# Kernel tuning notes

Hardware: AMD Instinct MI355X
Metric: run time of the kernel (lower is better)

Reference implementation:

```python
import jax, jax.numpy as jnp
import numpy as np

B, S, T = 16, 400, 51
V, E, H = 50000, 128, 256
MAX_OOV = 50
EXT = V + MAX_OOV
COV_LOSS_WEIGHT = 1.0


def setup_inputs() -> dict:
    key = jax.random.key(0)
    ks = jax.random.split(key, 24)
    sc = 0.05  # param scale
    inp = {
        "tgt": jax.random.randint(ks[0], (B, T), 0, V, dtype=jnp.int32),
        "hidden": jax.random.normal(ks[1], (1, B, H), jnp.float32),
        "cell": jax.random.normal(ks[2], (1, B, H), jnp.float32),
        "encoder_outputs": jax.random.normal(ks[3], (B, S, H), jnp.float32),
        "src_lens": jax.random.randint(ks[4], (B,), S // 2, S + 1, dtype=jnp.int32),
        "src_ids": jax.random.randint(ks[5], (B, S), 0, V, dtype=jnp.int32),
        # -1 means in-vocab token; >=0 means OOV slot index (max MAX_OOV-1)
        "src_oov_map": jax.random.randint(ks[6], (B, S), -1, MAX_OOV, dtype=jnp.int32),
        "embedding": jax.random.normal(ks[7], (V, E), jnp.float32) * sc,
        "W_h": jax.random.normal(ks[8], (H, H), jnp.float32) * sc,
        "W_s": jax.random.normal(ks[9], (H, H), jnp.float32) * sc,
        "w_c": jax.random.normal(ks[10], (H,), jnp.float32) * sc,
        "v": jax.random.normal(ks[11], (H,), jnp.float32) * sc,
        "b_attn": jnp.zeros((1,), jnp.float32),
        "W_ih": jax.random.normal(ks[12], (4 * H, E + H), jnp.float32) * sc,
        "W_hh": jax.random.normal(ks[13], (4 * H, H), jnp.float32) * sc,
        "b_ih": jax.random.normal(ks[14], (4 * H,), jnp.float32) * sc,
        "b_hh": jax.random.normal(ks[15], (4 * H,), jnp.float32) * sc,
        "W_pg": jax.random.normal(ks[16], (1, 2 * H + E), jnp.float32) * sc,
        "b_pg": jnp.zeros((1,), jnp.float32),
        "W_out": jax.random.normal(ks[17], (V, 2 * H), jnp.float32) * sc,
        "b_out": jnp.zeros((V,), jnp.float32),
    }
    return inp


def reference(tgt, hidden, cell, encoder_outputs, src_lens, src_ids, src_oov_map,
              embedding, W_h, W_s, w_c, v, b_attn,
              W_ih, W_hh, b_ih, b_hh, W_pg, b_pg, W_out, b_out):
    # Precompute encoder projection and masks (loop-invariant)
    Wh_h = jnp.einsum('bsh,kh->bsk', encoder_outputs, W_h)        # [B,S,H]
    pad_mask = jnp.arange(S)[None, :] >= src_lens[:, None]       # [B,S]
    copy_idx = jnp.where(src_oov_map >= 0, V + src_oov_map, src_ids)  # [B,S]
    batch_idx = jnp.arange(B)[:, None]

    def step(carry, y_prev):
        h, c, cov = carry                                       # [B,H],[B,H],[B,S]
        emb = embedding[y_prev]                                 # [B,E]
        # coverage attention (additive, See et al. 2017 eq. 9-11)
        attn_in = Wh_h + (h @ W_s.T)[:, None, :] + cov[..., None] * w_c + b_attn
        scores = jnp.tanh(attn_in) @ v                          # [B,S]
        scores = jnp.where(pad_mask, -1e9, scores)
        attn = jax.nn.softmax(scores, axis=1)                   # [B,S]
        context = jnp.einsum('bs,bsh->bh', attn, encoder_outputs)
        cov_loss = jnp.sum(jnp.minimum(attn, cov), axis=1)      # [B]
        # single-layer LSTM cell (torch gate order i,f,g,o)
        x = jnp.concatenate([emb, context], axis=1)             # [B,E+H]
        gates = x @ W_ih.T + h @ W_hh.T + b_ih + b_hh
        i, f, g, o = jnp.split(gates, 4, axis=1)
        c_new = jax.nn.sigmoid(f) * c + jax.nn.sigmoid(i) * jnp.tanh(g)
        h_new = jax.nn.sigmoid(o) * jnp.tanh(c_new)
        # pointer-generator mixture
        p_gen = jax.nn.sigmoid(
            jnp.concatenate([h_new, context, emb], axis=1) @ W_pg.T + b_pg)  # [B,1]
        logits = jnp.concatenate([h_new, context], axis=1) @ W_out.T + b_out
        vocab_dist = jax.nn.softmax(logits, axis=1)             # [B,V]
        ext_dist = jnp.pad(vocab_dist, ((0, 0), (0, MAX_OOV)))  # [B,EXT]
        copy_dist = jnp.zeros((B, EXT), vocab_dist.dtype).at[batch_idx, copy_idx].add(attn)
        final = p_gen * ext_dist + (1.0 - p_gen) * copy_dist
        return (h_new, c_new, cov + attn), (final, cov_loss)

    carry0 = (hidden[0], cell[0], jnp.zeros((B, S), jnp.float32))
    # teacher forcing: decoder input at step t is tgt[:, t-1], t = 1..T-1
    (hT, cT, _), (dists, cov_losses) = jax.lax.scan(step, carry0, tgt[:, :-1].T)
    all_dists = jnp.transpose(dists, (1, 0, 2))                 # [B,T-1,EXT]
    coverage_loss = COV_LOSS_WEIGHT * jnp.mean(cov_losses)
    return all_dists, hT[None], cT[None], coverage_loss
```

## Files before the change

### kernel.cpp

```cpp
#include <hip/hip_runtime.h>
#include <math.h>

#define CB 16
#define CS 400
#define CT 51
#define CTM1 50
#define CV 50000
#define CE 128
#define CH 256
#define CMAXOOV 50
#define CEXT (CV + CMAXOOV)
#define CX 640
#define NST 16
#define NGT 16
#define NWK 223
#define NBLK 256
#define NTILE 782

typedef __attribute__((ext_vector_type(4))) float f32x4;
typedef __attribute__((ext_vector_type(8))) short short8;
typedef unsigned int U32;
typedef unsigned long long U64;

__device__ __forceinline__ float wave_sum(float x) {
#pragma unroll
  for (int o = 32; o > 0; o >>= 1) x += __shfl_xor(x, o);
  return x;
}
__device__ __forceinline__ float sigm(float x) {
  return 1.f / (1.f + __expf(-x));
}
__device__ __forceinline__ float ftanh(float x) {
  x = fminf(fmaxf(x, -15.f), 15.f);
  float e = __expf(2.f * x);
  return (e - 1.f) / (e + 1.f);
}
__device__ __forceinline__ unsigned short f2bf(float f) {
  union { float f; U32 u; } x;
  x.f = f;
  U32 r = x.u + 0x7FFFu + ((x.u >> 16) & 1u);
  return (unsigned short)(r >> 16);
}
__device__ __forceinline__ float bf2f(unsigned short u) {
  return __uint_as_float(((U32)u) << 16);
}
__device__ __forceinline__ U64 pack4(float a, float b, float c, float d) {
  return (U64)f2bf(a) | ((U64)f2bf(b) << 16) | ((U64)f2bf(c) << 32) |
         ((U64)f2bf(d) << 48);
}
__device__ __forceinline__ U32 ald32(const U32* p) {
  return __hip_atomic_load(p, __ATOMIC_RELAXED, __HIP_MEMORY_SCOPE_AGENT);
}
__device__ __forceinline__ void ast32(U32* p, U32 v) {
  __hip_atomic_store(p, v, __ATOMIC_RELAXED, __HIP_MEMORY_SCOPE_AGENT);
}
__device__ __forceinline__ void ast64(U64* p, U64 v) {
  __hip_atomic_store(p, v, __ATOMIC_RELAXED, __HIP_MEMORY_SCOPE_AGENT);
}
#define VM0 asm volatile("s_waitcnt vmcnt(0)" ::: "memory")

__global__ __launch_bounds__(256) void pw_convert(
    const float* __restrict__ W, unsigned short* __restrict__ Wb) {
  size_t i = ((size_t)blockIdx.x * 256 + threadIdx.x) * 8;
  float4 a = *(const float4*)(W + i);
  float4 b = *(const float4*)(W + i + 4);
  short8 o;
  o[0] = (short)f2bf(a.x); o[1] = (short)f2bf(a.y);
  o[2] = (short)f2bf(a.z); o[3] = (short)f2bf(a.w);
  o[4] = (short)f2bf(b.x); o[5] = (short)f2bf(b.y);
  o[6] = (short)f2bf(b.z); o[7] = (short)f2bf(b.w);
  *(short8*)(Wb + i) = o;
}

__global__ __launch_bounds__(256) void pw_cat(
    const float* __restrict__ W_ih, const float* __restrict__ W_hh,
    unsigned short* __restrict__ Wcat) {
  int t8 = blockIdx.x * 256 + threadIdx.x;
  int j = t8 / 80, k8 = t8 % 80;
  short8 o;
#pragma unroll
  for (int i = 0; i < 8; ++i) {
    int k = k8 * 8 + i;
    float v = (k < CE + CH) ? W_ih[(size_t)j * (CE + CH) + k]
                            : W_hh[(size_t)j * CH + (k - (CE + CH))];
    o[i] = (short)f2bf(v);
  }
  *(short8*)(Wcat + (size_t)t8 * 8) = o;
}

__global__ __launch_bounds__(256) void pw_t256(const float* __restrict__ in,
                                               float* __restrict__ out) {
  int j = blockIdx.x, k = threadIdx.x;
  out[j * CH + k] = in[k * CH + j];
}

__global__ __launch_bounds__(256) void pw_t256_bf16(
    const float* __restrict__ in, unsigned short* __restrict__ out) {
  int j = blockIdx.x, k = threadIdx.x;
  out[j * CH + k] = f2bf(in[k * CH + j]);
}

__global__ __launch_bounds__(256) void pw_cvt16(
    const float* __restrict__ in, unsigned short* __restrict__ out) {
  size_t i = ((size_t)blockIdx.x * 256 + threadIdx.x) * 8;
  float4 a = *(const float4*)(in + i);
  float4 b = *(const float4*)(in + i + 4);
  short8 o;
  o[0] = (short)f2bf(a.x); o[1] = (short)f2bf(a.y);
  o[2] = (short)f2bf(a.z); o[3] = (short)f2bf(a.w);
  o[4] = (short)f2bf(b.x); o[5] = (short)f2bf(b.y);
  o[6] = (short)f2bf(b.z); o[7] = (short)f2bf(b.w);
  *(short8*)(out + i) = o;
}

__global__ __launch_bounds__(256) void p0_precompute(
    const float* __restrict__ enc, const float* __restrict__ W_hT,
    const int* __restrict__ src_ids, const int* __restrict__ src_oov,
    unsigned short* __restrict__ Wh_h16, int* __restrict__ copy_idx) {
  const int row0 = blockIdx.x * 8, tid = threadIdx.x;
  __shared__ float erT[CH * 8];
#pragma unroll
  for (int i = 0; i < 8; ++i) {
    int idx = tid + i * 256;
    int r = idx >> 8, j = idx & 255;
    erT[j * 8 + r] = enc[(size_t)row0 * CH + idx];
  }
  if (tid < 8) {
    int row = row0 + tid;
    int ov = src_oov[row];
    copy_idx[row] = (ov >= 0) ? (CV + ov) : src_ids[row];
  }
  __syncthreads();
  float acc[8] = {0, 0, 0, 0, 0, 0, 0, 0};
#pragma unroll 4
  for (int j = 0; j < CH; ++j) {
    float w = W_hT[j * CH + tid];
    float4 e0 = *(const float4*)&erT[j * 8];
    float4 e1 = *(const float4*)&erT[j * 8 + 4];
    acc[0] += e0.x * w; acc[1] += e0.y * w; acc[2] += e0.z * w; acc[3] += e0.w * w;
    acc[4] += e1.x * w; acc[5] += e1.y * w; acc[6] += e1.z * w; acc[7] += e1.w * w;
  }
#pragma unroll
  for (int r = 0; r < 8; ++r)
    Wh_h16[(size_t)(row0 + r) * CH + tid] = f2bf(acc[r]);
}

__global__ __launch_bounds__(256) void z_init(U32* __restrict__ ctrl,
                                              float* __restrict__ part) {
  int tid = blockIdx.x * 256 + threadIdx.x;
  if (tid < 2048) ctrl[tid] = 0u;
  for (int i = tid; i < CTM1 * CB * 64; i += 256 * 64) part[i] = 0.f;
}

__global__ __launch_bounds__(1024, 4) void mega(
    const int* __restrict__ tgt, const float* __restrict__ hidden,
    const float* __restrict__ cell, const int* __restrict__ src_lens,
    const float* __restrict__ embedding, const float* __restrict__ w_c,
    const float* __restrict__ v_vec, const float* __restrict__ b_attn,
    const float* __restrict__ b_ih, const float* __restrict__ b_hh,
    const float* __restrict__ W_pg, const float* __restrict__ b_pg,
    const float* __restrict__ b_out,
    const unsigned short* __restrict__ Wh_h16,
    const unsigned short* __restrict__ enc16,
    const unsigned short* __restrict__ W_sT16,
    const unsigned short* __restrict__ Wcat,
    const unsigned short* __restrict__ Wb, U64* __restrict__ A64,
    float* __restrict__ HexF, unsigned short* __restrict__ attn16,
    float* __restrict__ p_gen_g, float* __restrict__ part,
    float* __restrict__ covloss_b, U32* __restrict__ ctrl,
    float* __restrict__ dout) {
  const int bid = blockIdx.x, tid = threadIdx.x;
  const int lane = tid & 63, wv = tid >> 6;
  U32* release = ctrl + 256;
  U32* xrdy = ctrl + 1280;
  U32* grdy = ctrl + 1536;

  __shared__ __align__(16) U64 sh_big[2592];
  __shared__ float cov_s[CS];
  __shared__ float a_s[CS];
  __shared__ __align__(16) float h_cur[CH];
  __shared__ float hws_s[CH];
  __shared__ __align__(16) float ctx_s[CH];
  __shared__ float emb_s[CE];
  __shared__ float pctx[4 * CH];
  __shared__ float gsl[4][CB][16];
  __shared__ int sh_tok[CB];
  __shared__ float red[16];
  __shared__ float stat[4];
  __shared__ float prs[16][16];

  if (bid < NST) {
    const int b = bid;
    const int len = src_lens[b];
    const float ba = b_attn[0];
    const int k4 = lane * 4;
    const float4 wc4 = *(const float4*)(w_c + k4);
    const float4 vv4 = *(const float4*)(v_vec + k4);
    const int kg = tid & 255, grp = tid >> 8;
    float covl = 0.f;

    if (tid < CS) cov_s[tid] = 0.f;
    if (tid < CH) h_cur[tid] = hidden[b * CH + tid];
    __syncthreads();
    {
      float acc = 0.f;
#pragma unroll 8
      for (int j = grp * 64; j < grp * 64 + 64; ++j)
        acc += h_cur[j] * bf2f(W_sT16[j * CH + kg]);
      pctx[grp * CH + kg] = acc;
    }
    __syncthreads();
    if (tid < CH)
      hws_s[tid] = pctx[tid] + pctx[CH + tid] + pctx[2 * CH + tid] +
                   pctx[3 * CH + tid];
    __syncthreads();

    for (int t = 0; t < CTM1; ++t) {
      if (t > 0) {
        if (tid < CS) {
          float a = a_s[tid], cv = cov_s[tid];
          covl += fminf(a, cv);
          cov_s[tid] = cv + a;
        }
        __syncthreads();
      }
      float ps = 0.f;
      for (int s = wv; s < CS; s += 16) {
        float cv = cov_s[s];
        U64 wq = *(const U64*)(Wh_h16 + ((size_t)(b * CS + s)) * CH + k4);
        float p =
            ftanh(bf2f((unsigned short)wq) + hws_s[k4] + cv * wc4.x + ba) *
                vv4.x +
            ftanh(bf2f((unsigned short)(wq >> 16)) + hws_s[k4 + 1] +
                  cv * wc4.y + ba) *
                vv4.y +
            ftanh(bf2f((unsigned short)(wq >> 32)) + hws_s[k4 + 2] +
                  cv * wc4.z + ba) *
                vv4.z +
            ftanh(bf2f((unsigned short)(wq >> 48)) + hws_s[k4 + 3] +
                  cv * wc4.w + ba) *
                vv4.w;
        p = wave_sum(p);
        if (lane == 0) {
          float e = (s < len) ? __expf(p) : 0.f;
          a_s[s] = e;
          ps += e;
        }
      }
      if (lane == 0) red[wv] = ps;
      __syncthreads();
      if (tid == 0) {
        float s2 = 0.f;
#pragma unroll
        for (int i = 0; i < 16; ++i) s2 += red[i];
        stat[0] = 1.f / s2;
      }
      __syncthreads();
      const float inv = stat[0];
      if (tid < CS) {
        float a = a_s[tid] * inv;
        a_s[tid] = a;
        attn16[((size_t)t * CB + b) * CS + tid] = f2bf(a);
      }
      __syncthreads();
      {
        float pc = 0.f;
        const unsigned short* er =
            enc16 + ((size_t)(b * CS + grp * 100)) * CH + kg;
#pragma unroll 10
        for (int i = 0; i < 100; ++i)
          pc += a_s[grp * 100 + i] * bf2f(er[(size_t)i * CH]);
        pctx[grp * CH + kg] = pc;
      }
      __syncthreads();
      if (tid < CH)
        ctx_s[tid] = pctx[tid] + pctx[CH + tid] + pctx[2 * CH + tid] +
                     pctx[3 * CH + tid];
      __syncthreads();
      if (tid < 64) {
        ast64(&A64[(size_t)t * 2048 + b * 128 + 64 + tid],
              pack4(ctx_s[4 * tid], ctx_s[4 * tid + 1], ctx_s[4 * tid + 2],
                    ctx_s[4 * tid + 3]));
      }
      VM0;
      __syncthreads();
      if (tid == 0) ast32(&xrdy[b * 16], (U32)(t + 1));
      if (tid < CE)
        emb_s[tid] = embedding[(size_t)tgt[b * CT + t] * CE + tid];
      if (wv == 0) {
        int gg = 0;
        while (gg < (1 << 22)) {
          U32 v = (lane < NGT) ? ald32(&grdy[lane * 16]) : (U32)(t + 1);
          if (__all(v >= (U32)(t + 1))) break;
          __builtin_amdgcn_s_sleep(1);
          ++gg;
        }
      }
      __syncthreads();
      if (tid < CH) h_cur[tid] = HexF[((size_t)t * CB + b) * CH + tid];
      __syncthreads();
      {
        float acc = 0.f;
#pragma unroll 8
        for (int j = grp * 64; j < grp * 64 + 64; ++j)
          acc += h_cur[j] * bf2f(W_sT16[j * CH + kg]);
        pctx[grp * CH + kg] = acc;
      }
      __syncthreads();
      if (tid < CH)
        hws_s[tid] = pctx[tid] + pctx[CH + tid] + pctx[2 * CH + tid] +
                     pctx[3 * CH + tid];
      {
        float z = 0.f;
        if (tid < CH)
          z = h_cur[tid] * W_pg[tid] + ctx_s[tid] * W_pg[CH + tid];
        if (tid < CE) z += emb_s[tid] * W_pg[2 * CH + tid];
        z = wave_sum(z);
        if (lane == 0) red[wv] = z;
        __syncthreads();
        if (tid == 0) {
          float s2 = 0.f;
#pragma unroll
          for (int i = 0; i < 16; ++i) s2 += red[i];
          p_gen_g[t * CB + b] = sigm(s2 + b_pg[0]);
        }
      }
      __syncthreads();
    }
    if (tid < CS) covl += fminf(a_s[tid], cov_s[tid]);
    covl = wave_sum(covl);
    if (lane == 0) red[wv] = covl;
    __syncthreads();
    if (tid == 0) {
      float s2 = 0.f;
#pragma unroll
      for (int i = 0; i < 16; ++i) s2 += red[i];
      covloss_b[b] = s2;
    }
    if (tid < CH) {
      const size_t D0 = (size_t)CB * CTM1 * CEXT;
      dout[D0 + b * CH + tid] = h_cur[tid];
    }
  } else if (bid < NST + NGT) {
    const int g = bid - NST;
    const int nn = lane & 15, gq = lane >> 4;
    U64* xg64 = sh_big;
    short* xg_s = (short*)sh_big;
    const short8* x8 = (const short8*)sh_big;
    const int cb = tid >> 4, cj = tid & 15, cu = g * 16 + (tid & 15);
    float c_reg = 0.f, bi0 = 0.f, bi1 = 0.f, bi2 = 0.f, bi3 = 0.f;
    if (tid < 256) {
      c_reg = cell[cb * CH + cu];
      bi0 = b_ih[cu] + b_hh[cu];
      bi1 = b_ih[CH + cu] + b_hh[CH + cu];
      bi2 = b_ih[2 * CH + cu] + b_hh[2 * CH + cu];
      bi3 = b_ih[3 * CH + cu] + b_hh[3 * CH + cu];
    }
    for (int t = 0; t < CTM1; ++t) {
      if (t > 0 && wv == 0) {
        int gg = 0;
        while (gg < (1 << 22)) {
          U32 v = (lane < NGT) ? ald32(&grdy[lane * 16]) : (U32)t;
          if (__all(v >= (U32)t)) break;
          __builtin_amdgcn_s_sleep(1);
          ++gg;
        }
      }
      if (tid < CB) sh_tok[tid] = tgt[tid * CT + t];
      __syncthreads();
      for (int idx = tid; idx < CB * CE; idx += 1024) {
        int bb = idx >> 7, k = idx & 127;
        xg_s[bb * 648 + k] = (short)f2bf(embedding[(size_t)sh_tok[bb] * CE + k]);
      }
      if (t == 0) {
        for (int idx = tid; idx < CB * CH; idx += 1024) {
          int bb = idx >> 8, k = idx & 255;
          xg_s[bb * 648 + 384 + k] = (short)f2bf(hidden[bb * CH + k]);
        }
      } else {
        if (tid < 1024) {
          int bb = tid >> 6, i = tid & 63;
          xg64[bb * 162 + 96 + i] = A64[(size_t)(t - 1) * 2048 + bb * 128 + i];
        }
      }
      __syncthreads();
      f32x4 acc = {0.f, 0.f, 0.f, 0.f};
      if (wv < 4) {
        const int ncol = wv * 256 + g * 16 + nn;
        const short8* bp = (const short8*)Wcat + (size_t)ncol * 80;
#pragma unroll
        for (int kt = 0; kt < 4; ++kt)
          acc = __builtin_amdgcn_mfma_f32_16x16x32_bf16(
              x8[nn * 81 + kt * 4 + gq], bp[kt * 4 + gq], acc, 0, 0, 0);
#pragma unroll
        for (int kt = 12; kt < 20; ++kt)
          acc = __builtin_amdgcn_mfma_f32_16x16x32_bf16(
              x8[nn * 81 + kt * 4 + gq], bp[kt * 4 + gq], acc, 0, 0, 0);
      }
      if (wv == 0) {
        int gg = 0;
        while (gg < (1 << 22)) {
          U32 v = (lane < NST) ? ald32(&xrdy[lane * 16]) : (U32)(t + 1);
          if (__all(v >= (U32)(t + 1))) break;
          __builtin_amdgcn_s_sleep(1);
          ++gg;
        }
      }
      __syncthreads();
      if (tid < 1024) {
        int bb = tid >> 6, i = tid & 63;
        xg64[bb * 162 + 32 + i] = A64[(size_t)t * 2048 + bb * 128 + 64 + i];
      }
      __syncthreads();
      if (wv < 4) {
        const int ncol = wv * 256 + g * 16 + nn;
        const short8* bp = (const short8*)Wcat + (size_t)ncol * 80;
#pragma unroll
        for (int kt = 4; kt < 12; ++kt)
          acc = __builtin_amdgcn_mfma_f32_16x16x32_bf16(
              x8[nn * 81 + kt * 4 + gq], bp[kt * 4 + gq], acc, 0, 0, 0);
#pragma unroll
        for (int r = 0; r < 4; ++r) gsl[wv][gq * 4 + r][nn] = acc[r];
      }
      __syncthreads();
      if (tid < 256) {
        float gi = gsl[0][cb][cj] + bi0;
        float gf = gsl[1][cb][cj] + bi1;
        float gg2 = gsl[2][cb][cj] + bi2;
        float go = gsl[3][cb][cj] + bi3;
        float cn = sigm(gf) * c_reg + sigm(gi) * ftanh(gg2);
        c_reg = cn;
        float hn = sigm(go) * ftanh(cn);
        ast32((U32*)&HexF[((size_t)t * CB + cb) * CH + cu],
              __float_as_uint(hn));
        float h1 = __shfl_down(hn, 1);
        float h2 = __shfl_down(hn, 2);
        float h3 = __shfl_down(hn, 3);
        if (!(cj & 3))
          ast64(&A64[(size_t)t * 2048 + cb * 128 + (cu >> 2)],
                pack4(hn, h1, h2, h3));
      }
      VM0;
      __syncthreads();
      if (tid == 0) ast32(&grdy[g * 16], (U32)(t + 1));
    }
    if (tid < 256) {
      const size_t D0 = (size_t)CB * CTM1 * CEXT;
      dout[D0 + CB * CH + cb * CH + cu] = c_reg;
    }
  } else if (bid == NST + NGT) {
    for (int t = 0; t < CTM1; ++t) {
      if (wv == 0) {
        int gg = 0;
        while (gg < (1 << 22)) {
          U32 v = (lane < NGT) ? ald32(&grdy[lane * 16]) : (U32)(t + 1);
          if (__all(v >= (U32)(t + 1))) break;
          __builtin_amdgcn_s_sleep(4);
          ++gg;
        }
      }
      __syncthreads();
      if (tid < 64) ast32(&release[tid * 16], (U32)(t + 1));
      __syncthreads();
    }
  } else {
    const int vb = bid - NST - NGT - 1;
    const int rep = vb & 63;
    const int nn = lane & 15, g = lane >> 4;
    const int t4 = (wv >> 2) * NWK + vb;
    const int v = t4 * 64 + (wv & 3) * 16 + nn;
    const bool live = (t4 < NTILE) && (v < CV);
    const int vc = live ? v : CV - 1;
    U64* a64l = sh_big;
    const short8* lds8 = (const short8*)sh_big;
    const short8* bp = (const short8*)Wb + (size_t)vc * 64;
    const float bo = live ? b_out[v] : 0.f;
    for (int t = 0; t < CTM1; ++t) {
      if (tid == 0) {
        int gg = 0;
        while (ald32(&release[rep * 16]) < (U32)(t + 1) && ++gg < (1 << 18))
          __builtin_amdgcn_s_sleep(32);
      }
      __syncthreads();
      {
        const U64* src = A64 + (size_t)t * 2048;
#pragma unroll
        for (int i = 0; i < 2; ++i) {
          int idx = tid + i * 1024;
          int row = idx >> 7, col = idx & 127;
          a64l[row * 130 + col] = src[idx];
        }
      }
      __syncthreads();
      short8 af[16];
#pragma unroll
      for (int kt = 0; kt < 16; ++kt) af[kt] = lds8[nn * 65 + kt * 4 + g];
      f32x4 acc = {0.f, 0.f, 0.f, 0.f};
#pragma unroll
      for (int kt = 0; kt < 16; ++kt)
        acc = __builtin_amdgcn_mfma_f32_16x16x32_bf16(af[kt], bp[kt * 4 + g],
                                                      acc, 0, 0, 0);
      float ev[4];
#pragma unroll
      for (int r = 0; r < 4; ++r) {
        float e = live ? __expf(acc[r] + bo) : 0.f;
        if (live) dout[((size_t)((g * 4 + r) * CTM1 + t)) * CEXT + v] = e;
#pragma unroll
        for (int o = 1; o < 16; o <<= 1) e += __shfl_xor(e, o);
        ev[r] = e;
      }
      if (nn == 0) {
#pragma unroll
        for (int r = 0; r < 4; ++r) prs[wv][g * 4 + r] = ev[r];
      }
      __syncthreads();
      if (tid < 16) {
        float s = 0.f;
#pragma unroll
        for (int w = 0; w < 16; ++w) s += prs[w][tid];
        atomicAdd(&part[((size_t)t * CB + tid) * 64 + rep], s);
      }
      __syncthreads();
    }
  }
}

__global__ __launch_bounds__(256) void post_norm(
    const float* __restrict__ part, const float* __restrict__ p_gen_g,
    float* __restrict__ dout) {
  const int R = blockIdx.x;
  const int b = R / CTM1, t = R % CTM1;
  const int tid = threadIdx.x;
  __shared__ float stat;
  float s = (tid < 64) ? part[((size_t)t * CB + b) * 64 + tid] : 0.f;
  s = wave_sum(s);
  if (tid == 0) stat = p_gen_g[t * CB + b] / s;
  __syncthreads();
  float inv = stat;
  float* drow = dout + (size_t)R * CEXT;
  for (int v = tid; v < CEXT; v += 256)
    drow[v] = (v < CV) ? drow[v] * inv : 0.f;
}

__global__ __launch_bounds__(256) void post_tail(
    const unsigned short* __restrict__ attn16,
    const float* __restrict__ p_gen_g, const int* __restrict__ copy_idx,
    const float* __restrict__ covloss_b, float* __restrict__ dout) {
  const int b = blockIdx.x, tid = threadIdx.x;
  for (int t = 0; t < CTM1; ++t) {
    float pg1 = 1.f - p_gen_g[t * CB + b];
    const unsigned short* ar = attn16 + ((size_t)t * CB + b) * CS;
    float* drow = dout + ((size_t)(b * CTM1 + t)) * CEXT;
    for (int s = tid; s < CS; s += 256)
      atomicAdd(drow + copy_idx[b * CS + s], pg1 * bf2f(ar[s]));
  }
  if (b == 0 && tid == 0) {
    const size_t D0 = (size_t)CB * CTM1 * CEXT;
    float s = 0.f;
    for (int i = 0; i < CB; ++i) s += covloss_b[i];
    dout[D0 + 2 * CB * CH] = s / (float)(CTM1 * CB);
  }
}

extern "C" void kernel_launch(void* const* d_in, const int* in_sizes, int n_in,
                              void* d_out, int out_size, void* d_ws,
                              size_t ws_size, hipStream_t stream) {
  const int* tgt = (const int*)d_in[0];
  const float* hidden = (const float*)d_in[1];
  const float* cell = (const float*)d_in[2];
  const float* enc = (const float*)d_in[3];
  const int* src_lens = (const int*)d_in[4];
  const int* src_ids = (const int*)d_in[5];
  const int* src_oov = (const int*)d_in[6];
  const float* embedding = (const float*)d_in[7];
  const float* W_h = (const float*)d_in[8];
  const float* W_s = (const float*)d_in[9];
  const float* w_c = (const float*)d_in[10];
  const float* v_vec = (const float*)d_in[11];
  const float* b_attn = (const float*)d_in[12];
  const float* W_ih = (const float*)d_in[13];
  const float* W_hh = (const float*)d_in[14];
  const float* b_ih = (const float*)d_in[15];
  const float* b_hh = (const float*)d_in[16];
  const float* W_pg = (const float*)d_in[17];
  const float* b_pg = (const float*)d_in[18];
  const float* W_out = (const float*)d_in[19];
  const float* b_out = (const float*)d_in[20];
  float* dout = (float*)d_out;

  float* ws = (float*)d_ws;
  float* W_hT = ws;
  float* p_gen_g = W_hT + CH * CH;
  float* part = p_gen_g + CTM1 * CB;
  float* covloss_b = part + CTM1 * CB * 64;
  float* HexF = covloss_b + 16;
  int* copy_idx = (int*)(HexF + (size_t)CTM1 * CB * CH);
  U32* ctrl = (U32*)(copy_idx + CB * CS);
  U64* A64 = (U64*)(ctrl + 2048);
  unsigned short* attn16 =
      (unsigned short*)(A64 + (size_t)CTM1 * 2048);
  unsigned short* Wh_h16 = attn16 + (size_t)CTM1 * CB * CS;
  unsigned short* enc16 = Wh_h16 + (size_t)CB * CS * CH;
  unsigned short* W_sT16 = enc16 + (size_t)CB * CS * CH;
  unsigned short* Wcat = W_sT16 + CH * CH;
  unsigned short* Wb = Wcat + (size_t)(4 * CH) * CX;

  z_init<<<64, 256, 0, stream>>>(ctrl, part);
  pw_convert<<<(CV * 2 * CH) / (256 * 8), 256, 0, stream>>>(W_out, Wb);
  pw_cat<<<((4 * CH) * CX / 8) / 256, 256, 0, stream>>>(W_ih, W_hh, Wcat);
  pw_t256<<<CH, CH, 0, stream>>>(W_h, W_hT);
  pw_t256_bf16<<<CH, CH, 0, stream>>>(W_s, W_sT16);
  pw_cvt16<<<(CB * CS * CH) / (256 * 8), 256, 0, stream>>>(enc, enc16);
  p0_precompute<<<CB * CS / 8, 256, 0, stream>>>(enc, W_hT, src_ids, src_oov,
                                                 Wh_h16, copy_idx);

  void* kargs[] = {
      (void*)&tgt,      (void*)&hidden,    (void*)&cell,    (void*)&src_lens,
      (void*)&embedding,(void*)&w_c,       (void*)&v_vec,   (void*)&b_attn,
      (void*)&b_ih,     (void*)&b_hh,      (void*)&W_pg,    (void*)&b_pg,
      (void*)&b_out,    (void*)&Wh_h16,    (void*)&enc16,   (void*)&W_sT16,
      (void*)&Wcat,     (void*)&Wb,        (void*)&A64,     (void*)&HexF,
      (void*)&attn16,   (void*)&p_gen_g,   (void*)&part,    (void*)&covloss_b,
      (void*)&ctrl,     (void*)&dout};
  hipError_t e = hipLaunchCooperativeKernel((const void*)mega, dim3(NBLK),
                                            dim3(1024), kargs, 0, stream);
  if (e != hipSuccess) {
    hipLaunchKernelGGL(mega, dim3(NBLK), dim3(1024), 0, stream, tgt, hidden,
                       cell, src_lens, embedding, w_c, v_vec, b_attn, b_ih,
                       b_hh, W_pg, b_pg, b_out, Wh_h16, enc16, W_sT16, Wcat,
                       Wb, A64, HexF, attn16, p_gen_g, part, covloss_b, ctrl,
                       dout);
  }
  post_norm<<<CB * CTM1, 256, 0, stream>>>(part, p_gen_g, dout);
  post_tail<<<CB, 256, 0, stream>>>(attn16, p_gen_g, copy_idx, covloss_b,
                                    dout);
}
```

Before: 1.862 ms.

## Repartition LSTM gate blocks by batch group and move W_s projection into them

Each LSTM gate block now owns 4 batch rows and 64 hidden units, using all 16 waves for MFMA instead of 4. Each block computes partial h·W_s and h·W_pg products for its slice and publishes them, so attention blocks only sum four partials instead of redoing a 256x256 matvec on the serial critical path. Attention blocks also wait only on the 4 gate blocks that own their batch group rather than on all 16. The cost is extra global traffic for the partial buffers and more per-step work inside the gate blocks.

```diff
diff --git a/kernel.cpp b/kernel.cpp
--- a/kernel.cpp
+++ b/kernel.cpp
@@ -54,6 +54,10 @@
 __device__ __forceinline__ void ast32(U32* p, U32 v) {
   __hip_atomic_store(p, v, __ATOMIC_RELAXED, __HIP_MEMORY_SCOPE_AGENT);
 }
+__device__ __forceinline__ void astf(float* p, float v) {
+  __hip_atomic_store((U32*)p, __float_as_uint(v), __ATOMIC_RELAXED,
+                     __HIP_MEMORY_SCOPE_AGENT);
+}
 __device__ __forceinline__ void ast64(U64* p, U64 v) {
   __hip_atomic_store(p, v, __ATOMIC_RELAXED, __HIP_MEMORY_SCOPE_AGENT);
 }
@@ -165,7 +169,8 @@
     const unsigned short* __restrict__ W_sT16,
     const unsigned short* __restrict__ Wcat,
     const unsigned short* __restrict__ Wb, U64* __restrict__ A64,
-    float* __restrict__ HexF, unsigned short* __restrict__ attn16,
+    float* __restrict__ HexF, float* __restrict__ HwsP,
+    float* __restrict__ PgP, unsigned short* __restrict__ attn16,
     float* __restrict__ p_gen_g, float* __restrict__ part,
     float* __restrict__ covloss_b, U32* __restrict__ ctrl,
     float* __restrict__ dout) {
@@ -183,7 +188,7 @@
   __shared__ __align__(16) float ctx_s[CH];
   __shared__ float emb_s[CE];
   __shared__ float pctx[4 * CH];
-  __shared__ float gsl[4][CB][16];
+  __shared__ float gsl[4][4][64];
   __shared__ int sh_tok[CB];
   __shared__ float red[16];
   __shared__ float stat[4];
@@ -191,6 +196,7 @@
 
   if (bid < NST) {
     const int b = bid;
+    const int gi = b >> 2;
     const int len = src_lens[b];
     const float ba = b_attn[0];
     const int k4 = lane * 4;
@@ -276,6 +282,8 @@
       if (tid < CH)
         ctx_s[tid] = pctx[tid] + pctx[CH + tid] + pctx[2 * CH + tid] +
                      pctx[3 * CH + tid];
+      if (tid < CE)
+        emb_s[tid] = embedding[(size_t)tgt[b * CT + t] * CE + tid];
       __syncthreads();
       if (tid < 64) {
         ast64(&A64[(size_t)t * 2048 + b * 128 + 64 + tid],
@@ -285,45 +293,36 @@
       VM0;
       __syncthreads();
       if (tid == 0) ast32(&xrdy[b * 16], (U32)(t + 1));
-      if (tid < CE)
-        emb_s[tid] = embedding[(size_t)tgt[b * CT + t] * CE + tid];
+      {
+        float z = 0.f;
+        if (tid < CH) z = ctx_s[tid] * W_pg[CH + tid];
+        if (tid < CE) z += emb_s[tid] * W_pg[2 * CH + tid];
+        z = wave_sum(z);
+        if (lane == 0) red[wv] = z;
+      }
+      __syncthreads();
       if (wv == 0) {
         int gg = 0;
         while (gg < (1 << 22)) {
-          U32 v = (lane < NGT) ? ald32(&grdy[lane * 16]) : (U32)(t + 1);
+          U32 v = (lane < 4) ? ald32(&grdy[(gi * 4 + lane) * 16])
+                             : (U32)(t + 1);
           if (__all(v >= (U32)(t + 1))) break;
           __builtin_amdgcn_s_sleep(1);
           ++gg;
         }
       }
       __syncthreads();
-      if (tid < CH) h_cur[tid] = HexF[((size_t)t * CB + b) * CH + tid];
-      __syncthreads();
-      {
-        float acc = 0.f;
-#pragma unroll 8
-        for (int j = grp * 64; j < grp * 64 + 64; ++j)
-          acc += h_cur[j] * bf2f(W_sT16[j * CH + kg]);
-        pctx[grp * CH + kg] = acc;
-      }
-      __syncthreads();
-      if (tid < CH)
-        hws_s[tid] = pctx[tid] + pctx[CH + tid] + pctx[2 * CH + tid] +
-                     pctx[3 * CH + tid];
-      {
-        float z = 0.f;
-        if (tid < CH)
-          z = h_cur[tid] * W_pg[tid] + ctx_s[tid] * W_pg[CH + tid];
-        if (tid < CE) z += emb_s[tid] * W_pg[2 * CH + tid];
-        z = wave_sum(z);
-        if (lane == 0) red[wv] = z;
-        __syncthreads();
-        if (tid == 0) {
-          float s2 = 0.f;
-#pragma unroll
-          for (int i = 0; i < 16; ++i) s2 += red[i];
-          p_gen_g[t * CB + b] = sigm(s2 + b_pg[0]);
-        }
+      if (tid < CH) {
+        const float* hp = HwsP + (((size_t)t * CB + b) * 4) * CH + tid;
+        hws_s[tid] = hp[0] + hp[CH] + hp[2 * CH] + hp[3 * CH];
+      }
+      if (tid == 0) {
+        float s2 = 0.f;
+#pragma unroll
+        for (int i = 0; i < 16; ++i) s2 += red[i];
+        const float* pp = PgP + ((size_t)t * CB + b) * 4;
+        s2 += pp[0] + pp[1] + pp[2] + pp[3];
+        p_gen_g[t * CB + b] = sigm(s2 + b_pg[0]);
       }
       __syncthreads();
     }
@@ -339,55 +338,60 @@
     }
     if (tid < CH) {
       const size_t D0 = (size_t)CB * CTM1 * CEXT;
-      dout[D0 + b * CH + tid] = h_cur[tid];
+      dout[D0 + b * CH + tid] = HexF[((size_t)49 * CB + b) * CH + tid];
     }
   } else if (bid < NST + NGT) {
     const int g = bid - NST;
+    const int gi = g >> 2, gj = g & 3;
+    const int b0 = gi * 4, u0 = gj * 64;
     const int nn = lane & 15, gq = lane >> 4;
     U64* xg64 = sh_big;
     short* xg_s = (short*)sh_big;
     const short8* x8 = (const short8*)sh_big;
-    const int cb = tid >> 4, cj = tid & 15, cu = g * 16 + (tid & 15);
+    const int g2 = wv >> 2;
+    const int ncol = g2 * 256 + u0 + (wv & 3) * 16 + nn;
+    const short8* bp = (const short8*)Wcat + (size_t)ncol * 80;
+    const int cbL = wv, cu = lane;
     float c_reg = 0.f, bi0 = 0.f, bi1 = 0.f, bi2 = 0.f, bi3 = 0.f;
-    if (tid < 256) {
-      c_reg = cell[cb * CH + cu];
-      bi0 = b_ih[cu] + b_hh[cu];
-      bi1 = b_ih[CH + cu] + b_hh[CH + cu];
-      bi2 = b_ih[2 * CH + cu] + b_hh[2 * CH + cu];
-      bi3 = b_ih[3 * CH + cu] + b_hh[3 * CH + cu];
+    if (wv < 4) {
+      c_reg = cell[(b0 + cbL) * CH + u0 + cu];
+      bi0 = b_ih[u0 + cu] + b_hh[u0 + cu];
+      bi1 = b_ih[CH + u0 + cu] + b_hh[CH + u0 + cu];
+      bi2 = b_ih[2 * CH + u0 + cu] + b_hh[2 * CH + u0 + cu];
+      bi3 = b_ih[3 * CH + u0 + cu] + b_hh[3 * CH + u0 + cu];
     }
     for (int t = 0; t < CTM1; ++t) {
       if (t > 0 && wv == 0) {
         int gg = 0;
         while (gg < (1 << 22)) {
-          U32 v = (lane < NGT) ? ald32(&grdy[lane * 16]) : (U32)t;
+          U32 v = (lane < 4) ? ald32(&grdy[(gi * 4 + lane) * 16]) : (U32)t;
           if (__all(v >= (U32)t)) break;
           __builtin_amdgcn_s_sleep(1);
           ++gg;
         }
       }
-      if (tid < CB) sh_tok[tid] = tgt[tid * CT + t];
-      __syncthreads();
-      for (int idx = tid; idx < CB * CE; idx += 1024) {
-        int bb = idx >> 7, k = idx & 127;
-        xg_s[bb * 648 + k] = (short)f2bf(embedding[(size_t)sh_tok[bb] * CE + k]);
+      if (tid < 4) sh_tok[tid] = tgt[(b0 + tid) * CT + t];
+      __syncthreads();
+      if (tid < 512) {
+        int bb = tid >> 7, k = tid & 127;
+        xg_s[bb * 648 + k] =
+            (short)f2bf(embedding[(size_t)sh_tok[bb] * CE + k]);
       }
       if (t == 0) {
-        for (int idx = tid; idx < CB * CH; idx += 1024) {
-          int bb = idx >> 8, k = idx & 255;
-          xg_s[bb * 648 + 384 + k] = (short)f2bf(hidden[bb * CH + k]);
+        if (tid < 1024) {
+          int bb = tid >> 8, k = tid & 255;
+          xg_s[bb * 648 + 384 + k] = (short)f2bf(hidden[(b0 + bb) * CH + k]);
         }
       } else {
-        if (tid < 1024) {
-          int bb = tid >> 6, i = tid & 63;
-          xg64[bb * 162 + 96 + i] = A64[(size_t)(t - 1) * 2048 + bb * 128 + i];
+        if (tid < 256) {
+          int bb = tid >> 6, iu = tid & 63;
+          xg64[bb * 162 + 96 + iu] =
+              A64[(size_t)(t - 1) * 2048 + (b0 + bb) * 128 + iu];
         }
       }
       __syncthreads();
       f32x4 acc = {0.f, 0.f, 0.f, 0.f};
-      if (wv < 4) {
-        const int ncol = wv * 256 + g * 16 + nn;
-        const short8* bp = (const short8*)Wcat + (size_t)ncol * 80;
+      {
 #pragma unroll
         for (int kt = 0; kt < 4; ++kt)
           acc = __builtin_amdgcn_mfma_f32_16x16x32_bf16(
@@ -400,53 +404,71 @@
       if (wv == 0) {
         int gg = 0;
         while (gg < (1 << 22)) {
-          U32 v = (lane < NST) ? ald32(&xrdy[lane * 16]) : (U32)(t + 1);
+          U32 v = (lane < 4) ? ald32(&xrdy[(b0 + lane) * 16]) : (U32)(t + 1);
           if (__all(v >= (U32)(t + 1))) break;
           __builtin_amdgcn_s_sleep(1);
           ++gg;
         }
       }
       __syncthreads();
-      if (tid < 1024) {
-        int bb = tid >> 6, i = tid & 63;
-        xg64[bb * 162 + 32 + i] = A64[(size_t)t * 2048 + bb * 128 + 64 + i];
-      }
-      __syncthreads();
-      if (wv < 4) {
-        const int ncol = wv * 256 + g * 16 + nn;
-        const short8* bp = (const short8*)Wcat + (size_t)ncol * 80;
+      if (tid < 256) {
+        int bb = tid >> 6, iu = tid & 63;
+        xg64[bb * 162 + 32 + iu] =
+            A64[(size_t)t * 2048 + (b0 + bb) * 128 + 64 + iu];
+      }
+      __syncthreads();
+      {
 #pragma unroll
         for (int kt = 4; kt < 12; ++kt)
           acc = __builtin_amdgcn_mfma_f32_16x16x32_bf16(
               x8[nn * 81 + kt * 4 + gq], bp[kt * 4 + gq], acc, 0, 0, 0);
-#pragma unroll
-        for (int r = 0; r < 4; ++r) gsl[wv][gq * 4 + r][nn] = acc[r];
-      }
-      __syncthreads();
-      if (tid < 256) {
-        float gi = gsl[0][cb][cj] + bi0;
-        float gf = gsl[1][cb][cj] + bi1;
-        float gg2 = gsl[2][cb][cj] + bi2;
-        float go = gsl[3][cb][cj] + bi3;
-        float cn = sigm(gf) * c_reg + sigm(gi) * ftanh(gg2);
+        if (gq == 0) {
+#pragma unroll
+          for (int r = 0; r < 4; ++r)
+            gsl[g2][r][(wv & 3) * 16 + nn] = acc[r];
+        }
+      }
+      __syncthreads();
+      if (wv < 4) {
+        float gi_ = gsl[0][cbL][cu] + bi0;
+        float gf = gsl[1][cbL][cu] + bi1;
+        float gg2 = gsl[2][cbL][cu] + bi2;
+        float go = gsl[3][cbL][cu] + bi3;
+        float cn = sigm(gf) * c_reg + sigm(gi_) * ftanh(gg2);
         c_reg = cn;
         float hn = sigm(go) * ftanh(cn);
-        ast32((U32*)&HexF[((size_t)t * CB + cb) * CH + cu],
-              __float_as_uint(hn));
+        h_cur[cbL * 64 + cu] = hn;
+        astf(&HexF[((size_t)t * CB + b0 + cbL) * CH + u0 + cu], hn);
         float h1 = __shfl_down(hn, 1);
         float h2 = __shfl_down(hn, 2);
         float h3 = __shfl_down(hn, 3);
-        if (!(cj & 3))
-          ast64(&A64[(size_t)t * 2048 + cb * 128 + (cu >> 2)],
+        if (!(cu & 3))
+          ast64(&A64[(size_t)t * 2048 + (b0 + cbL) * 128 + gj * 16 +
+                     (cu >> 2)],
                 pack4(hn, h1, h2, h3));
       }
+      __syncthreads();
+      {
+        int bb = tid >> 8, k = tid & 255;
+        float acc2 = 0.f;
+#pragma unroll 8
+        for (int u = 0; u < 64; ++u)
+          acc2 += h_cur[bb * 64 + u] * bf2f(W_sT16[(u0 + u) * CH + k]);
+        astf(&HwsP[(((size_t)t * CB + b0 + bb) * 4 + gj) * CH + k], acc2);
+      }
+      if (wv < 4) {
+        float pp = h_cur[cbL * 64 + cu] * W_pg[u0 + cu];
+        pp = wave_sum(pp);
+        if (cu == 0)
+          astf(&PgP[((size_t)t * CB + b0 + cbL) * 4 + gj], pp);
+      }
       VM0;
       __syncthreads();
       if (tid == 0) ast32(&grdy[g * 16], (U32)(t + 1));
     }
-    if (tid < 256) {
+    if (wv < 4) {
       const size_t D0 = (size_t)CB * CTM1 * CEXT;
-      dout[D0 + CB * CH + cb * CH + cu] = c_reg;
+      dout[D0 + CB * CH + (b0 + cbL) * CH + u0 + cu] = c_reg;
     }
   } else if (bid == NST + NGT) {
     for (int t = 0; t < CTM1; ++t) {
@@ -594,7 +616,9 @@
   float* part = p_gen_g + CTM1 * CB;
   float* covloss_b = part + CTM1 * CB * 64;
   float* HexF = covloss_b + 16;
-  int* copy_idx = (int*)(HexF + (size_t)CTM1 * CB * CH);
+  float* HwsP = HexF + (size_t)CTM1 * CB * CH;
+  float* PgP = HwsP + (size_t)CTM1 * CB * 4 * CH;
+  int* copy_idx = (int*)(PgP + CTM1 * CB * 4);
   U32* ctrl = (U32*)(copy_idx + CB * CS);
   U64* A64 = (U64*)(ctrl + 2048);
   unsigned short* attn16 =
@@ -620,16 +644,16 @@
       (void*)&b_ih,     (void*)&b_hh,      (void*)&W_pg,    (void*)&b_pg,
       (void*)&b_out,    (void*)&Wh_h16,    (void*)&enc16,   (void*)&W_sT16,
       (void*)&Wcat,     (void*)&Wb,        (void*)&A64,     (void*)&HexF,
-      (void*)&attn16,   (void*)&p_gen_g,   (void*)&part,    (void*)&covloss_b,
-      (void*)&ctrl,     (void*)&dout};
+      (void*)&HwsP,     (void*)&PgP,       (void*)&attn16,  (void*)&p_gen_g,
+      (void*)&part,     (void*)&covloss_b, (void*)&ctrl,    (void*)&dout};
   hipError_t e = hipLaunchCooperativeKernel((const void*)mega, dim3(NBLK),
                                             dim3(1024), kargs, 0, stream);
   if (e != hipSuccess) {
     hipLaunchKernelGGL(mega, dim3(NBLK), dim3(1024), 0, stream, tgt, hidden,
                        cell, src_lens, embedding, w_c, v_vec, b_attn, b_ih,
                        b_hh, W_pg, b_pg, b_out, Wh_h16, enc16, W_sT16, Wcat,
-                       Wb, A64, HexF, attn16, p_gen_g, part, covloss_b, ctrl,
-                       dout);
+                       Wb, A64, HexF, HwsP, PgP, attn16, p_gen_g, part,
+                       covloss_b, ctrl, dout);
   }
   post_norm<<<CB * CTM1, 256, 0, stream>>>(part, p_gen_g, dout);
   post_tail<<<CB, 256, 0, stream>>>(attn16, p_gen_g, copy_idx, covloss_b,
```

Result: slower. 2.105 ms (+13.0%).
